# Kernel optimization log

Hardware: AMD Instinct MI355X
Metric: run time of the kernel (lower is better)

## Reference

```python
import jax, jax.numpy as jnp
import numpy as np

N = 50000
E = 800000
G = 256          # number of graphs in the batch
F_IN = 128
H1, D1 = 12, 32  # conv1: heads, out-per-head (concat -> 384)
H2, D2 = 1, 64   # conv2: single head
NEG_SLOPE = 0.2


def setup_inputs() -> dict:
    key = jax.random.key(0)
    ks = jax.random.split(key, 12)
    x = jax.random.normal(ks[0], (N, F_IN), dtype=jnp.float32)
    edge_index = jax.random.randint(ks[1], (2, E), 0, N, dtype=jnp.int64)
    batch = jnp.sort(jax.random.randint(ks[2], (N,), 0, G, dtype=jnp.int64))
    # conv1 params (Glorot-ish scaling)
    W1 = jax.random.normal(ks[3], (F_IN, H1 * D1), dtype=jnp.float32) * (1.0 / np.sqrt(F_IN))
    att_src1 = jax.random.normal(ks[4], (H1, D1), dtype=jnp.float32) * (1.0 / np.sqrt(D1))
    att_dst1 = jax.random.normal(ks[5], (H1, D1), dtype=jnp.float32) * (1.0 / np.sqrt(D1))
    bias1 = jnp.zeros((H1 * D1,), dtype=jnp.float32)
    # conv2 params
    W2 = jax.random.normal(ks[6], (H1 * D1, H2 * D2), dtype=jnp.float32) * (1.0 / np.sqrt(H1 * D1))
    att_src2 = jax.random.normal(ks[7], (H2, D2), dtype=jnp.float32) * (1.0 / np.sqrt(D2))
    att_dst2 = jax.random.normal(ks[8], (H2, D2), dtype=jnp.float32) * (1.0 / np.sqrt(D2))
    bias2 = jnp.zeros((H2 * D2,), dtype=jnp.float32)
    return {"x": x, "edge_index": edge_index, "batch": batch,
            "W1": W1, "att_src1": att_src1, "att_dst1": att_dst1, "bias1": bias1,
            "W2": W2, "att_src2": att_src2, "att_dst2": att_dst2, "bias2": bias2}


def gat_conv(x, src, dst, W, att_src, att_dst, bias, heads, d_out):
    # x: [N, F] -> h: [N, heads, d_out]
    h = (x @ W).reshape(N, heads, d_out)
    # per-node attention halves: [N, heads]
    a_src = jnp.einsum('nhd,hd->nh', h, att_src)
    a_dst = jnp.einsum('nhd,hd->nh', h, att_dst)
    # per-edge logits (edges include self-loops): [Etot, heads]
    e = jax.nn.leaky_relu(a_src[src] + a_dst[dst], NEG_SLOPE)
    # segment softmax over incoming edges of each destination node
    m = jax.ops.segment_max(e, dst, num_segments=N)          # [N, heads]
    e = jnp.exp(e - m[dst])
    s = jax.ops.segment_sum(e, dst, num_segments=N)          # [N, heads]
    alpha = e / s[dst]
    # weighted aggregation: [N, heads, d_out]
    out = jax.ops.segment_sum(alpha[:, :, None] * h[src], dst, num_segments=N)
    return out.reshape(N, heads * d_out) + bias


def reference(x, edge_index, batch, W1, att_src1, att_dst1, bias1,
              W2, att_src2, att_dst2, bias2):
    # add self-loops (PyG GATConv default add_self_loops=True)
    loops = jnp.arange(N, dtype=edge_index.dtype)
    src = jnp.concatenate([edge_index[0], loops])
    dst = jnp.concatenate([edge_index[1], loops])

    h = jax.nn.relu(gat_conv(x, src, dst, W1, att_src1, att_dst1, bias1, H1, D1))
    h = gat_conv(h, src, dst, W2, att_src2, att_dst2, bias2, H2, D2)

    # global mean pool over graphs
    sums = jax.ops.segment_sum(h, batch, num_segments=G)                 # [G, 64]
    cnts = jax.ops.segment_sum(jnp.ones((N,), h.dtype), batch, num_segments=G)
    return sums / jnp.maximum(cnts, 1.0)[:, None]
```

## Files before the change

kernel.cpp:

```cpp
#include <hip/hip_runtime.h>

#define N_NODES 50000
#define N_EDGES 800000
#define ETOT (N_EDGES + N_NODES)
#define G_GRAPHS 256
#define F_IN 128
#define H1 12
#define D1 32
#define C1 (H1*D1)
#define C2 64
#define NEG 0.2f
#define SCAN_B 1024
#define NBLK_SCAN ((N_NODES + SCAN_B - 1)/SCAN_B)

using bf16x8  = __attribute__((ext_vector_type(8))) short;
using ushort8 = __attribute__((ext_vector_type(8))) unsigned short;
using f32x4   = __attribute__((ext_vector_type(4))) float;

__device__ __forceinline__ float lrelu(float x){ return x > 0.f ? x : NEG*x; }
__device__ __forceinline__ unsigned short f2bf(float f){
  unsigned u = __float_as_uint(f);
  u += 0x7fffu + ((u >> 16) & 1u);
  return (unsigned short)(u >> 16);
}
__device__ __forceinline__ float bf2f(unsigned short h){
  return __uint_as_float(((unsigned)h) << 16);
}
__device__ __forceinline__ float wexp(float l){ return __expf(fminf(l, 30.f)); }

#define B_CAST ((N_NODES*F_IN/4 + 255)/256)
#define B_W1   ((F_IN*C1 + 255)/256)
#define B_W2   ((C1*C2 + 255)/256)
#define B_WAB  ((32*F_IN + 255)/256)
__global__ void prep_kernel(const float* __restrict__ x, const float* __restrict__ W1,
    const float* __restrict__ W2, const float* __restrict__ att_src,
    const float* __restrict__ att_dst, unsigned short* __restrict__ xb,
    unsigned short* __restrict__ w1t, unsigned short* __restrict__ w2t,
    unsigned short* __restrict__ wAb){
  int b = blockIdx.x, tid = threadIdx.x;
  if (b < B_CAST){
    int base = (b*256 + tid)*4;
    if (base >= N_NODES*F_IN) return;
    float4 v = *(const float4*)(x + base);
    ushort4 o; o.x=f2bf(v.x); o.y=f2bf(v.y); o.z=f2bf(v.z); o.w=f2bf(v.w);
    *(ushort4*)(xb + base) = o;
  } else if (b < B_CAST + B_W1){
    int i = (b - B_CAST)*256 + tid;
    if (i >= F_IN*C1) return;
    int n = i / F_IN, k = i % F_IN;
    w1t[i] = f2bf(W1[(size_t)k*C1 + n]);
  } else if (b < B_CAST + B_W1 + B_W2){
    int i = (b - B_CAST - B_W1)*256 + tid;
    if (i >= C1*C2) return;
    int n = i / C1, k = i % C1;
    w2t[i] = f2bf(W2[(size_t)k*C2 + n]);
  } else {
    int i = (b - B_CAST - B_W1 - B_W2)*256 + tid;
    if (i >= 32*F_IN) return;
    int c = i >> 7, k = i & 127;
    float v = 0.f;
    if (c < 12){
      #pragma unroll
      for (int dd=0; dd<D1; ++dd) v += W1[(size_t)k*C1 + c*D1 + dd] * att_src[c*D1 + dd];
    } else if (c < 24){
      int h = c - 12;
      #pragma unroll
      for (int dd=0; dd<D1; ++dd) v += W1[(size_t)k*C1 + h*D1 + dd] * att_dst[h*D1 + dd];
    }
    wAb[i] = f2bf(v);
  }
}

template<int BM,int BN,int WM,int WN,bool F32OUT>
__global__ __launch_bounds__(256) void gemm_mfma(const unsigned short* __restrict__ A,
    const unsigned short* __restrict__ Bt, void* __restrict__ Cv,
    int M, int N, int K){
  constexpr int BK = 32;
  __shared__ unsigned short As2[4][BM][8];
  __shared__ unsigned short Bs2[4][BN][8];
  const int tid  = threadIdx.x;
  const int wid  = tid >> 6, lane = tid & 63;
  constexpr int NWX = BN / WN;
  const int wrow = (wid / NWX) * WM, wcol = (wid % NWX) * WN;
  constexpr int MR = WM/16, NR = WN/16;
  const int row0 = blockIdx.x * BM, col0 = blockIdx.y * BN;
  const int r = lane & 15, koct = lane >> 4;
  f32x4 acc[MR][NR];
  #pragma unroll
  for (int m=0;m<MR;m++)
    #pragma unroll
    for (int n=0;n<NR;n++) acc[m][n] = f32x4{0.f,0.f,0.f,0.f};

  for (int k0 = 0; k0 < K; k0 += BK){
    for (int s = tid; s < BM*8; s += 256){
      int rr = s >> 3, cc = (s & 7) * 4;
      int gr = row0 + rr;
      ushort4 v = (gr < M) ? *(const ushort4*)(A + (size_t)gr*K + k0 + cc)
                           : ushort4{0,0,0,0};
      *(ushort4*)(&As2[cc>>3][rr][cc&7]) = v;
    }
    for (int s = tid; s < BN*8; s += 256){
      int rr = s >> 3, cc = (s & 7) * 4;
      ushort4 v = *(const ushort4*)(Bt + (size_t)(col0+rr)*K + k0 + cc);
      *(ushort4*)(&Bs2[cc>>3][rr][cc&7]) = v;
    }
    __syncthreads();
    bf16x8 af[MR], bq[NR];
    #pragma unroll
    for (int m=0;m<MR;m++) af[m] = *(const bf16x8*)(&As2[koct][wrow + m*16 + r][0]);
    #pragma unroll
    for (int n=0;n<NR;n++) bq[n] = *(const bf16x8*)(&Bs2[koct][wcol + n*16 + r][0]);
    #pragma unroll
    for (int m=0;m<MR;m++)
      #pragma unroll
      for (int n=0;n<NR;n++)
        acc[m][n] = __builtin_amdgcn_mfma_f32_16x16x32_bf16(af[m], bq[n], acc[m][n], 0,0,0);
    __syncthreads();
  }
  #pragma unroll
  for (int m=0;m<MR;m++){
    #pragma unroll
    for (int rr=0; rr<4; rr++){
      int grow = row0 + wrow + m*16 + koct*4 + rr;
      if (grow < M){
        #pragma unroll
        for (int n=0;n<NR;n++){
          if constexpr (F32OUT)
            ((float*)Cv)[(size_t)grow*N + col0 + wcol + n*16 + r] = acc[m][n][rr];
          else
            ((unsigned short*)Cv)[(size_t)grow*N + col0 + wcol + n*16 + r] = f2bf(acc[m][n][rr]);
        }
      }
    }
  }
}

#define EGRID ((ETOT + 255)/256)
#define NGRID ((N_NODES + 255)/256)
__global__ void count_cnt_kernel(const int* __restrict__ ei, const int* __restrict__ batch,
                                 int* __restrict__ counts, int* __restrict__ cnt){
  if ((int)blockIdx.x < EGRID){
    int e = blockIdx.x*256 + threadIdx.x;
    if (e >= ETOT) return;
    int d = (e < N_EDGES) ? ei[N_EDGES + e] : (e - N_EDGES);
    atomicAdd(&counts[d], 1);
  } else {
    int n = (blockIdx.x - EGRID)*256 + threadIdx.x;
    if (n < N_NODES) atomicAdd(&cnt[batch[n]], 1);
  }
}
__global__ __launch_bounds__(SCAN_B) void scan_pass1(const int* __restrict__ counts,
    int* __restrict__ excl, int* __restrict__ bsum){
  __shared__ int sdata[SCAN_B];
  int i = blockIdx.x*SCAN_B + threadIdx.x;
  int v = (i < N_NODES) ? counts[i] : 0;
  sdata[threadIdx.x] = v;
  __syncthreads();
  for (int off=1; off<SCAN_B; off<<=1){
    int t = (threadIdx.x >= off) ? sdata[threadIdx.x-off] : 0;
    __syncthreads();
    sdata[threadIdx.x] += t;
    __syncthreads();
  }
  if (i < N_NODES) excl[i] = sdata[threadIdx.x] - v;
  if (threadIdx.x == SCAN_B-1) bsum[blockIdx.x] = sdata[SCAN_B-1];
}
__global__ void scan_pass3(int* __restrict__ rowptr, const int* __restrict__ bsum,
                           int* __restrict__ cursor){
  __shared__ int carry_s;
  int sblk = blockIdx.x >> 2;
  if (threadIdx.x == 0){
    int c = 0;
    for (int b=0; b<sblk; ++b) c += bsum[b];
    carry_s = c;
  }
  __syncthreads();
  int i = blockIdx.x*256 + (int)threadIdx.x;
  if (i < N_NODES){
    int r = rowptr[i] + carry_s;
    rowptr[i] = r; cursor[i] = r;
  }
  if (i == N_NODES) rowptr[N_NODES] = ETOT;
}
__global__ void scatter_kernel(const int* __restrict__ ei, int* __restrict__ cursor,
                               int* __restrict__ csr_src, int* __restrict__ csr_dst){
  int e = blockIdx.x*blockDim.x + threadIdx.x;
  if (e >= ETOT) return;
  int s, d;
  if (e < N_EDGES){ s = ei[e]; d = ei[N_EDGES + e]; } else { s = d = e - N_EDGES; }
  int slot = atomicAdd(&cursor[d], 1);
  csr_src[slot] = s;
  csr_dst[slot] = d;
}

__global__ void wprep_kernel(const int* __restrict__ csr, const int* __restrict__ csrd,
                             const float* __restrict__ asd, unsigned short* __restrict__ walpha){
  int j = blockIdx.x*256 + threadIdx.x;
  if (j >= ETOT) return;
  int s = csr[j], d = csrd[j];
  float4 s0 = *(const float4*)(asd + (size_t)s*32);
  float4 s1 = *(const float4*)(asd + (size_t)s*32 + 4);
  float4 s2 = *(const float4*)(asd + (size_t)s*32 + 8);
  float4 d0 = *(const float4*)(asd + (size_t)d*32 + 12);
  float4 d1 = *(const float4*)(asd + (size_t)d*32 + 16);
  float4 d2 = *(const float4*)(asd + (size_t)d*32 + 20);
  float as[12] = {s0.x,s0.y,s0.z,s0.w, s1.x,s1.y,s1.z,s1.w, s2.x,s2.y,s2.z,s2.w};
  float ad[12] = {d0.x,d0.y,d0.z,d0.w, d1.x,d1.y,d1.z,d1.w, d2.x,d2.y,d2.z,d2.w};
  unsigned short wb[12];
  #pragma unroll
  for (int h=0;h<12;h++) wb[h] = f2bf(wexp(lrelu(as[h] + ad[h])));
  unsigned short* wp = walpha + (size_t)j*12;
  *(ushort4*)(wp)   = ushort4{wb[0],wb[1],wb[2],wb[3]};
  *(ushort4*)(wp+4) = ushort4{wb[4],wb[5],wb[6],wb[7]};
  *(ushort4*)(wp+8) = ushort4{wb[8],wb[9],wb[10],wb[11]};
}

__global__ __launch_bounds__(256) void agg1g_kernel(const int* __restrict__ rowptr,
    const int* __restrict__ csr, const unsigned short* __restrict__ xb,
    const unsigned short* __restrict__ walpha, const unsigned short* __restrict__ w1t,
    const unsigned short* __restrict__ w2t, const float* __restrict__ bias1,
    const float* __restrict__ att_src2, const float* __restrict__ att_dst2,
    unsigned short* __restrict__ h2, float* __restrict__ asrc2, float* __restrict__ adst2){
  constexpr int ROWE = 6*F_IN + 8;
  constexpr int WROW = 16*12 + 4;
  constexpr int ROWR = 192 + 8;
  __shared__ unsigned short agg[16*ROWE];
  __shared__ float wlds[16][WROW];

  unsigned short* reluLDS = (unsigned short*)&wlds[0][0];
  float* red = (float*)&agg[0];

  const int tid  = threadIdx.x;
  const int slot = tid >> 4;
  const int t16  = tid & 15;
  const int base = ((tid & 63) >> 4) * 16;
  const int d    = blockIdx.x*16 + slot;
  const int r0 = rowptr[d], r1 = rowptr[d+1];

  float acc[12][8];
  #pragma unroll
  for (int h=0;h<12;h++)
    #pragma unroll
    for (int i=0;i<8;i++) acc[h][i] = 0.f;
  float ss[12];
  #pragma unroll
  for (int h=0;h<12;h++) ss[h] = 0.f;

  for (int c0 = r0; c0 < r1; c0 += 16){
    int nc = min(16, r1 - c0);
    int s_st = 0;
    if (t16 < nc){
      int j = c0 + t16;
      s_st = csr[j];
      const unsigned short* wp = walpha + (size_t)j*12;
      ushort4 u0 = *(const ushort4*)(wp);
      ushort4 u1 = *(const ushort4*)(wp+4);
      ushort4 u2 = *(const ushort4*)(wp+8);
      float w[12] = {bf2f(u0.x),bf2f(u0.y),bf2f(u0.z),bf2f(u0.w),
                     bf2f(u1.x),bf2f(u1.y),bf2f(u1.z),bf2f(u1.w),
                     bf2f(u2.x),bf2f(u2.y),bf2f(u2.z),bf2f(u2.w)};
      #pragma unroll
      for (int h=0;h<12;h++) ss[h] += w[h];
      *(float4*)(&wlds[slot][t16*12 + 0]) = float4{w[0],w[1],w[2],w[3]};
      *(float4*)(&wlds[slot][t16*12 + 4]) = float4{w[4],w[5],w[6],w[7]};
      *(float4*)(&wlds[slot][t16*12 + 8]) = float4{w[8],w[9],w[10],w[11]};
    }
    __builtin_amdgcn_wave_barrier();
    int sA = __shfl(s_st, base + 0);
    ushort8 xA = *(const ushort8*)(xb + (size_t)sA*F_IN + t16*8);
    ushort8 xB = {0,0,0,0,0,0,0,0}, xC = {0,0,0,0,0,0,0,0};
    if (nc > 1){
      int sB = __shfl(s_st, base + 1);
      xB = *(const ushort8*)(xb + (size_t)sB*F_IN + t16*8);
    }
    if (nc > 2){
      int sC = __shfl(s_st, base + 2);
      xC = *(const ushort8*)(xb + (size_t)sC*F_IN + t16*8);
    }
    for (int e = 0; e < nc; ++e){
      ushort8 cx = xA;
      xA = xB; xB = xC;
      if (e + 3 < nc){
        int sN = __shfl(s_st, base + e + 3);
        xC = *(const ushort8*)(xb + (size_t)sN*F_IN + t16*8);
      }
      float4 w0 = *(const float4*)(&wlds[slot][e*12 + 0]);
      float4 w1 = *(const float4*)(&wlds[slot][e*12 + 4]);
      float4 w2 = *(const float4*)(&wlds[slot][e*12 + 8]);
      float xf[8];
      #pragma unroll
      for (int i=0;i<8;i++) xf[i] = bf2f((unsigned short)cx[i]);
      float w[12] = {w0.x,w0.y,w0.z,w0.w, w1.x,w1.y,w1.z,w1.w, w2.x,w2.y,w2.z,w2.w};
      #pragma unroll
      for (int h=0;h<12;h++)
        #pragma unroll
        for (int i=0;i<8;i++) acc[h][i] += w[h]*xf[i];
    }
    __builtin_amdgcn_wave_barrier();
  }

  #pragma unroll
  for (int h=0;h<12;h++){
    #pragma unroll
    for (int off=8; off; off>>=1) ss[h] += __shfl_xor(ss[h], off);
  }
  float inv[12];
  #pragma unroll
  for (int h=0;h<12;h++) inv[h] = 1.f / ss[h];

  const int wv = tid >> 6, wl = tid & 63;
  const int er = wl & 15, eq = wl >> 4;
  f32x4 h2acc = {0.f,0.f,0.f,0.f};
  #pragma unroll
  for (int hf = 0; hf < 2; ++hf){
    __syncthreads();
    #pragma unroll
    for (int h = 0; h < 6; ++h){
      int hh = hf*6 + h;
      ushort8 v;
      #pragma unroll
      for (int i=0;i<8;i++) v[i] = f2bf(acc[hh][i]*inv[hh]);
      *(ushort8*)(&agg[slot*ROWE + h*F_IN + t16*8]) = v;
    }
    __syncthreads();
    for (int tt = wv; tt < 12; tt += 4){
      int h = tt >> 1, nb = tt & 1;
      int hh = hf*6 + h;
      f32x4 c = {0.f,0.f,0.f,0.f};
      #pragma unroll
      for (int kk=0; kk<4; ++kk){
        bf16x8 af = *(const bf16x8*)(&agg[er*ROWE + h*F_IN + kk*32 + eq*8]);
        bf16x8 bq = *(const bf16x8*)(w1t + (size_t)(hh*32 + nb*16 + er)*F_IN + kk*32 + eq*8);
        c = __builtin_amdgcn_mfma_f32_16x16x32_bf16(af, bq, c, 0,0,0);
      }
      int lcol = tt*16 + er;
      float bv = bias1[hf*192 + lcol];
      #pragma unroll
      for (int rr=0; rr<4; ++rr){
        int row = eq*4 + rr;
        reluLDS[row*ROWR + lcol] = f2bf(fmaxf(c[rr] + bv, 0.f));
      }
    }
    __syncthreads();
    #pragma unroll
    for (int kk=0; kk<6; ++kk){
      bf16x8 af = *(const bf16x8*)(&reluLDS[er*ROWR + kk*32 + eq*8]);
      bf16x8 bq = *(const bf16x8*)(w2t + (size_t)(wv*16 + er)*C1 + hf*192 + kk*32 + eq*8);
      h2acc = __builtin_amdgcn_mfma_f32_16x16x32_bf16(af, bq, h2acc, 0,0,0);
    }
  }
  __syncthreads();

  float attS = att_src2[wv*16 + er];
  float attD = att_dst2[wv*16 + er];
  float psum[4], pdum[4];
  #pragma unroll
  for (int rr=0; rr<4; ++rr){
    int row = eq*4 + rr;
    int gn = blockIdx.x*16 + row;
    h2[(size_t)gn*C2 + wv*16 + er] = f2bf(h2acc[rr]);
    psum[rr] = h2acc[rr]*attS;
    pdum[rr] = h2acc[rr]*attD;
  }
  #pragma unroll
  for (int rr=0; rr<4; ++rr){
    #pragma unroll
    for (int off=8; off; off>>=1){
      psum[rr] += __shfl_xor(psum[rr], off);
      pdum[rr] += __shfl_xor(pdum[rr], off);
    }
  }
  if (er == 0){
    #pragma unroll
    for (int rr=0; rr<4; ++rr){
      int row = eq*4 + rr;
      red[(wv*16 + row)*2 + 0] = psum[rr];
      red[(wv*16 + row)*2 + 1] = pdum[rr];
    }
  }
  __syncthreads();
  if (tid < 32){
    int row = tid >> 1, which = tid & 1;
    float v = red[row*2+which] + red[(16+row)*2+which] + red[(32+row)*2+which] + red[(48+row)*2+which];
    int gn = blockIdx.x*16 + row;
    if (which == 0) asrc2[gn] = v; else adst2[gn] = v;
  }
}

__global__ __launch_bounds__(256) void agg2s_kernel(const int* __restrict__ rowptr,
    const int* __restrict__ csr, const unsigned short* __restrict__ h2,
    const float* __restrict__ asrc, const float* __restrict__ adst,
    const float* __restrict__ bias, const int* __restrict__ batch,
    float* __restrict__ pool){
  const int tid  = threadIdx.x;
  const int slot = tid >> 4;
  const int t16  = tid & 15;
  const int base = ((tid & 63) >> 4) * 16;
  const int d    = blockIdx.x*16 + slot;
  const int r0 = rowptr[d], r1 = rowptr[d+1];
  const float ad = adst[d];

  float ssp = 0.f;
  float a0=0.f, a1=0.f, a2=0.f, a3=0.f;

  for (int c0 = r0; c0 < r1; c0 += 16){
    int nc = min(16, r1 - c0);
    int s_st = 0; float w_st = 0.f;
    if (t16 < nc){
      s_st = csr[c0 + t16];
      w_st = wexp(lrelu(asrc[s_st] + ad));
      ssp += w_st;
    }
    int sA = __shfl(s_st, base + 0);
    ushort4 xA = *(const ushort4*)(h2 + (size_t)sA*C2 + t16*4);
    ushort4 xB = {0,0,0,0}, xC = {0,0,0,0};
    if (nc > 1){
      int sB = __shfl(s_st, base + 1);
      xB = *(const ushort4*)(h2 + (size_t)sB*C2 + t16*4);
    }
    if (nc > 2){
      int sC = __shfl(s_st, base + 2);
      xC = *(const ushort4*)(h2 + (size_t)sC*C2 + t16*4);
    }
    for (int e = 0; e < nc; ++e){
      ushort4 cx = xA;
      xA = xB; xB = xC;
      if (e + 3 < nc){
        int sN = __shfl(s_st, base + e + 3);
        xC = *(const ushort4*)(h2 + (size_t)sN*C2 + t16*4);
      }
      float w = __shfl(w_st, base + e);
      a0 += w*bf2f(cx.x);
      a1 += w*bf2f(cx.y);
      a2 += w*bf2f(cx.z);
      a3 += w*bf2f(cx.w);
    }
  }
  #pragma unroll
  for (int off=8; off; off>>=1) ssp += __shfl_xor(ssp, off);
  float inv = 1.f / ssp;
  int g = batch[d];
  int fb = t16*4;
  atomicAdd(&pool[g*C2 + fb+0], a0*inv + bias[fb+0]);
  atomicAdd(&pool[g*C2 + fb+1], a1*inv + bias[fb+1]);
  atomicAdd(&pool[g*C2 + fb+2], a2*inv + bias[fb+2]);
  atomicAdd(&pool[g*C2 + fb+3], a3*inv + bias[fb+3]);
}

__global__ void finalize_kernel(const float* __restrict__ sums, const int* __restrict__ cnt,
                                float* __restrict__ out){
  int i = blockIdx.x*blockDim.x + threadIdx.x;
  if (i >= G_GRAPHS*C2) return;
  int g = i >> 6;
  out[i] = sums[i] / fmaxf((float)cnt[g], 1.f);
}

extern "C" void kernel_launch(void* const* d_in, const int* in_sizes, int n_in,
                              void* d_out, int out_size, void* d_ws, size_t ws_size,
                              hipStream_t stream) {
  const float* x        = (const float*)d_in[0];
  const int*   ei       = (const int*)  d_in[1];
  const int*   batch    = (const int*)  d_in[2];
  const float* W1       = (const float*)d_in[3];
  const float* att_src1 = (const float*)d_in[4];
  const float* att_dst1 = (const float*)d_in[5];
  const float* bias1    = (const float*)d_in[6];
  const float* W2       = (const float*)d_in[7];
  const float* att_src2 = (const float*)d_in[8];
  const float* att_dst2 = (const float*)d_in[9];
  const float* bias2    = (const float*)d_in[10];
  float* out = (float*)d_out;

  char* ws = (char*)d_ws;
  size_t o = 0;
  auto alloc = [&](size_t bytes)->size_t{ size_t r=o; o=(o+bytes+255)&~(size_t)255; return r; };

  size_t xb_o     = alloc((size_t)N_NODES*F_IN*2);
  size_t w1t_o    = alloc((size_t)C1*F_IN*2);
  size_t w2t_o    = alloc((size_t)C2*C1*2);
  size_t wab_o    = alloc((size_t)32*F_IN*2);
  size_t asd_o    = alloc((size_t)N_NODES*32*4);
  size_t h2_o     = alloc((size_t)N_NODES*C2*2);
  size_t asrc2_o  = alloc((size_t)N_NODES*4);
  size_t adst2_o  = alloc((size_t)N_NODES*4);
  size_t walpha_o = alloc((size_t)ETOT*12*2);
  size_t zero_beg = o;
  size_t counts_o = alloc((size_t)N_NODES*4);
  size_t pool_o   = alloc((size_t)G_GRAPHS*C2*4);
  size_t cnt_o    = alloc((size_t)G_GRAPHS*4);
  size_t zero_end = o;
  size_t rowptr_o = alloc((size_t)(N_NODES+1)*4);
  size_t bsum_o   = alloc((size_t)NBLK_SCAN*4);
  size_t cursor_o = alloc((size_t)N_NODES*4);
  size_t csr_o    = alloc((size_t)ETOT*4);
  size_t csrd_o   = alloc((size_t)ETOT*4);

  unsigned short* xb    = (unsigned short*)(ws + xb_o);
  unsigned short* w1t   = (unsigned short*)(ws + w1t_o);
  unsigned short* w2t   = (unsigned short*)(ws + w2t_o);
  unsigned short* wab   = (unsigned short*)(ws + wab_o);
  float* asd    = (float*)(ws + asd_o);
  unsigned short* h2b   = (unsigned short*)(ws + h2_o);
  float* asrc2  = (float*)(ws + asrc2_o);
  float* adst2  = (float*)(ws + adst2_o);
  unsigned short* walpha = (unsigned short*)(ws + walpha_o);
  int*   counts = (int*)  (ws + counts_o);
  float* poolf  = (float*)(ws + pool_o);
  int*   cnt    = (int*)  (ws + cnt_o);
  int*   rowptr = (int*)  (ws + rowptr_o);
  int*   bsum   = (int*)  (ws + bsum_o);
  int*   cursor = (int*)  (ws + cursor_o);
  int*   csrsrc = (int*)  (ws + csr_o);
  int*   csrdst = (int*)  (ws + csrd_o);

  hipMemsetAsync(ws + zero_beg, 0, zero_end - zero_beg, stream);

  const int TPB = 256;

  prep_kernel<<<B_CAST + B_W1 + B_W2 + B_WAB, TPB, 0, stream>>>(
      x, W1, W2, att_src1, att_dst1, xb, w1t, w2t, wab);

  count_cnt_kernel<<<EGRID + NGRID, TPB, 0, stream>>>(ei, batch, counts, cnt);
  scan_pass1<<<NBLK_SCAN, SCAN_B, 0, stream>>>(counts, rowptr, bsum);
  scan_pass3<<<(N_NODES + 1 + 255)/256, TPB, 0, stream>>>(rowptr, bsum, cursor);
  scatter_kernel<<<EGRID, TPB, 0, stream>>>(ei, cursor, csrsrc, csrdst);

  gemm_mfma<64,32,32,16,true><<<dim3((N_NODES+63)/64, 1), 256, 0, stream>>>(xb, wab, asd, N_NODES, 32, F_IN);
  wprep_kernel<<<EGRID, TPB, 0, stream>>>(csrsrc, csrdst, asd, walpha);
  agg1g_kernel<<<N_NODES/16, TPB, 0, stream>>>(rowptr, csrsrc, xb, walpha, w1t, w2t,
                                               bias1, att_src2, att_dst2, h2b, asrc2, adst2);
  agg2s_kernel<<<(N_NODES+15)/16, TPB, 0, stream>>>(rowptr, csrsrc, h2b, asrc2, adst2, bias2, batch, poolf);

  finalize_kernel<<<(G_GRAPHS*C2 + TPB-1)/TPB, TPB, 0, stream>>>(poolf, cnt, out);
}
```

Before: 418.7 us.

## Use 32 lanes per destination node in layer-1 aggregation with 512-thread blocks

The layer-1 aggregation kernel now assigns 32 lanes per destination node instead of 16. Each lane holds 4 features, so the accumulator shrinks from 12x8 to 12x4 registers, and edges are processed in chunks of 32. The block doubles to 512 threads (8 waves) with launch bounds requesting higher occupancy, and the MFMA epilogue is restricted to 4 waves. This is meant to cut register pressure and raise memory-level parallelism for the gather, at the cost of narrower 8-byte loads and idle waves during the epilogue.

```diff
diff --git a/kernel.cpp b/kernel.cpp
--- a/kernel.cpp
+++ b/kernel.cpp
@@ -215,14 +215,14 @@
   *(ushort4*)(wp+8) = ushort4{wb[8],wb[9],wb[10],wb[11]};
 }
 
-__global__ __launch_bounds__(256) void agg1g_kernel(const int* __restrict__ rowptr,
+__global__ __launch_bounds__(512, 4) void agg1h_kernel(const int* __restrict__ rowptr,
     const int* __restrict__ csr, const unsigned short* __restrict__ xb,
     const unsigned short* __restrict__ walpha, const unsigned short* __restrict__ w1t,
     const unsigned short* __restrict__ w2t, const float* __restrict__ bias1,
     const float* __restrict__ att_src2, const float* __restrict__ att_dst2,
     unsigned short* __restrict__ h2, float* __restrict__ asrc2, float* __restrict__ adst2){
   constexpr int ROWE = 6*F_IN + 8;
-  constexpr int WROW = 16*12 + 4;
+  constexpr int WROW = 32*12 + 4;
   constexpr int ROWR = 192 + 8;
   __shared__ unsigned short agg[16*ROWE];
   __shared__ float wlds[16][WROW];
@@ -231,26 +231,29 @@
   float* red = (float*)&agg[0];
 
   const int tid  = threadIdx.x;
-  const int slot = tid >> 4;
-  const int t16  = tid & 15;
-  const int base = ((tid & 63) >> 4) * 16;
+  const int wv   = tid >> 6;
+  const int lane = tid & 63;
+  const int half = lane >> 5;
+  const int t32  = lane & 31;
+  const int base = lane & 32;
+  const int slot = wv*2 + half;
   const int d    = blockIdx.x*16 + slot;
   const int r0 = rowptr[d], r1 = rowptr[d+1];
 
-  float acc[12][8];
+  float acc[12][4];
   #pragma unroll
   for (int h=0;h<12;h++)
     #pragma unroll
-    for (int i=0;i<8;i++) acc[h][i] = 0.f;
+    for (int i=0;i<4;i++) acc[h][i] = 0.f;
   float ss[12];
   #pragma unroll
   for (int h=0;h<12;h++) ss[h] = 0.f;
 
-  for (int c0 = r0; c0 < r1; c0 += 16){
-    int nc = min(16, r1 - c0);
+  for (int c0 = r0; c0 < r1; c0 += 32){
+    int nc = min(32, r1 - c0);
     int s_st = 0;
-    if (t16 < nc){
-      int j = c0 + t16;
+    if (t32 < nc){
+      int j = c0 + t32;
       s_st = csr[j];
       const unsigned short* wp = walpha + (size_t)j*12;
       ushort4 u0 = *(const ushort4*)(wp);
@@ -261,40 +264,38 @@
                      bf2f(u2.x),bf2f(u2.y),bf2f(u2.z),bf2f(u2.w)};
       #pragma unroll
       for (int h=0;h<12;h++) ss[h] += w[h];
-      *(float4*)(&wlds[slot][t16*12 + 0]) = float4{w[0],w[1],w[2],w[3]};
-      *(float4*)(&wlds[slot][t16*12 + 4]) = float4{w[4],w[5],w[6],w[7]};
-      *(float4*)(&wlds[slot][t16*12 + 8]) = float4{w[8],w[9],w[10],w[11]};
+      *(float4*)(&wlds[slot][t32*12 + 0]) = float4{w[0],w[1],w[2],w[3]};
+      *(float4*)(&wlds[slot][t32*12 + 4]) = float4{w[4],w[5],w[6],w[7]};
+      *(float4*)(&wlds[slot][t32*12 + 8]) = float4{w[8],w[9],w[10],w[11]};
     }
     __builtin_amdgcn_wave_barrier();
     int sA = __shfl(s_st, base + 0);
-    ushort8 xA = *(const ushort8*)(xb + (size_t)sA*F_IN + t16*8);
-    ushort8 xB = {0,0,0,0,0,0,0,0}, xC = {0,0,0,0,0,0,0,0};
+    ushort4 xA = *(const ushort4*)(xb + (size_t)sA*F_IN + t32*4);
+    ushort4 xB = {0,0,0,0}, xC = {0,0,0,0};
     if (nc > 1){
       int sB = __shfl(s_st, base + 1);
-      xB = *(const ushort8*)(xb + (size_t)sB*F_IN + t16*8);
+      xB = *(const ushort4*)(xb + (size_t)sB*F_IN + t32*4);
     }
     if (nc > 2){
       int sC = __shfl(s_st, base + 2);
-      xC = *(const ushort8*)(xb + (size_t)sC*F_IN + t16*8);
+      xC = *(const ushort4*)(xb + (size_t)sC*F_IN + t32*4);
     }
     for (int e = 0; e < nc; ++e){
-      ushort8 cx = xA;
+      ushort4 cx = xA;
       xA = xB; xB = xC;
       if (e + 3 < nc){
         int sN = __shfl(s_st, base + e + 3);
-        xC = *(const ushort8*)(xb + (size_t)sN*F_IN + t16*8);
+        xC = *(const ushort4*)(xb + (size_t)sN*F_IN + t32*4);
       }
       float4 w0 = *(const float4*)(&wlds[slot][e*12 + 0]);
       float4 w1 = *(const float4*)(&wlds[slot][e*12 + 4]);
       float4 w2 = *(const float4*)(&wlds[slot][e*12 + 8]);
-      float xf[8];
-      #pragma unroll
-      for (int i=0;i<8;i++) xf[i] = bf2f((unsigned short)cx[i]);
+      float xf[4] = {bf2f(cx.x), bf2f(cx.y), bf2f(cx.z), bf2f(cx.w)};
       float w[12] = {w0.x,w0.y,w0.z,w0.w, w1.x,w1.y,w1.z,w1.w, w2.x,w2.y,w2.z,w2.w};
       #pragma unroll
       for (int h=0;h<12;h++)
         #pragma unroll
-        for (int i=0;i<8;i++) acc[h][i] += w[h]*xf[i];
+        for (int i=0;i<4;i++) acc[h][i] += w[h]*xf[i];
     }
     __builtin_amdgcn_wave_barrier();
   }
@@ -302,14 +303,13 @@
   #pragma unroll
   for (int h=0;h<12;h++){
     #pragma unroll
-    for (int off=8; off; off>>=1) ss[h] += __shfl_xor(ss[h], off);
+    for (int off=16; off; off>>=1) ss[h] += __shfl_xor(ss[h], off);
   }
   float inv[12];
   #pragma unroll
   for (int h=0;h<12;h++) inv[h] = 1.f / ss[h];
 
-  const int wv = tid >> 6, wl = tid & 63;
-  const int er = wl & 15, eq = wl >> 4;
+  const int er = lane & 15, eq = lane >> 4;
   f32x4 h2acc = {0.f,0.f,0.f,0.f};
   #pragma unroll
   for (int hf = 0; hf < 2; ++hf){
@@ -317,13 +317,13 @@
     #pragma unroll
     for (int h = 0; h < 6; ++h){
       int hh = hf*6 + h;
-      ushort8 v;
-      #pragma unroll
-      for (int i=0;i<8;i++) v[i] = f2bf(acc[hh][i]*inv[hh]);
-      *(ushort8*)(&agg[slot*ROWE + h*F_IN + t16*8]) = v;
-    }
-    __syncthreads();
-    for (int tt = wv; tt < 12; tt += 4){
+      ushort4 v;
+      v.x = f2bf(acc[hh][0]*inv[hh]); v.y = f2bf(acc[hh][1]*inv[hh]);
+      v.z = f2bf(acc[hh][2]*inv[hh]); v.w = f2bf(acc[hh][3]*inv[hh]);
+      *(ushort4*)(&agg[slot*ROWE + h*F_IN + t32*4]) = v;
+    }
+    __syncthreads();
+    for (int tt = wv; tt < 12; tt += 8){
       int h = tt >> 1, nb = tt & 1;
       int hh = hf*6 + h;
       f32x4 c = {0.f,0.f,0.f,0.f};
@@ -342,40 +342,44 @@
       }
     }
     __syncthreads();
-    #pragma unroll
-    for (int kk=0; kk<6; ++kk){
-      bf16x8 af = *(const bf16x8*)(&reluLDS[er*ROWR + kk*32 + eq*8]);
-      bf16x8 bq = *(const bf16x8*)(w2t + (size_t)(wv*16 + er)*C1 + hf*192 + kk*32 + eq*8);
-      h2acc = __builtin_amdgcn_mfma_f32_16x16x32_bf16(af, bq, h2acc, 0,0,0);
+    if (wv < 4){
+      #pragma unroll
+      for (int kk=0; kk<6; ++kk){
+        bf16x8 af = *(const bf16x8*)(&reluLDS[er*ROWR + kk*32 + eq*8]);
+        bf16x8 bq = *(const bf16x8*)(w2t + (size_t)(wv*16 + er)*C1 + hf*192 + kk*32 + eq*8);
+        h2acc = __builtin_amdgcn_mfma_f32_16x16x32_bf16(af, bq, h2acc, 0,0,0);
+      }
     }
   }
   __syncthreads();
 
-  float attS = att_src2[wv*16 + er];
-  float attD = att_dst2[wv*16 + er];
-  float psum[4], pdum[4];
-  #pragma unroll
-  for (int rr=0; rr<4; ++rr){
-    int row = eq*4 + rr;
-    int gn = blockIdx.x*16 + row;
-    h2[(size_t)gn*C2 + wv*16 + er] = f2bf(h2acc[rr]);
-    psum[rr] = h2acc[rr]*attS;
-    pdum[rr] = h2acc[rr]*attD;
-  }
-  #pragma unroll
-  for (int rr=0; rr<4; ++rr){
-    #pragma unroll
-    for (int off=8; off; off>>=1){
-      psum[rr] += __shfl_xor(psum[rr], off);
-      pdum[rr] += __shfl_xor(pdum[rr], off);
-    }
-  }
-  if (er == 0){
+  if (wv < 4){
+    float attS = att_src2[wv*16 + er];
+    float attD = att_dst2[wv*16 + er];
+    float psum[4], pdum[4];
     #pragma unroll
     for (int rr=0; rr<4; ++rr){
       int row = eq*4 + rr;
-      red[(wv*16 + row)*2 + 0] = psum[rr];
-      red[(wv*16 + row)*2 + 1] = pdum[rr];
+      int gn = blockIdx.x*16 + row;
+      h2[(size_t)gn*C2 + wv*16 + er] = f2bf(h2acc[rr]);
+      psum[rr] = h2acc[rr]*attS;
+      pdum[rr] = h2acc[rr]*attD;
+    }
+    #pragma unroll
+    for (int rr=0; rr<4; ++rr){
+      #pragma unroll
+      for (int off=8; off; off>>=1){
+        psum[rr] += __shfl_xor(psum[rr], off);
+        pdum[rr] += __shfl_xor(pdum[rr], off);
+      }
+    }
+    if (er == 0){
+      #pragma unroll
+      for (int rr=0; rr<4; ++rr){
+        int row = eq*4 + rr;
+        red[(wv*16 + row)*2 + 0] = psum[rr];
+        red[(wv*16 + row)*2 + 1] = pdum[rr];
+      }
     }
   }
   __syncthreads();
@@ -527,7 +531,7 @@
 
   gemm_mfma<64,32,32,16,true><<<dim3((N_NODES+63)/64, 1), 256, 0, stream>>>(xb, wab, asd, N_NODES, 32, F_IN);
   wprep_kernel<<<EGRID, TPB, 0, stream>>>(csrsrc, csrdst, asd, walpha);
-  agg1g_kernel<<<N_NODES/16, TPB, 0, stream>>>(rowptr, csrsrc, xb, walpha, w1t, w2t,
+  agg1h_kernel<<<N_NODES/16, 512, 0, stream>>>(rowptr, csrsrc, xb, walpha, w1t, w2t,
                                                bias1, att_src2, att_dst2, h2b, asrc2, adst2);
   agg2s_kernel<<<(N_NODES+15)/16, TPB, 0, stream>>>(rowptr, csrsrc, h2b, asrc2, adst2, bias2, batch, poolf);
 
```

New measurement: 415.0 us, median of 2. No clear change (-0.9%).
